# Kernel optimization log

Measured on AMD Instinct MI355X. Metric: run time of the kernel, lower is better.

## Reference

```python
import jax, jax.numpy as jnp
import numpy as np

N_HEAD = 16
NEG_INF = -1e30


def sparsemax(z):
    # sparsemax over last axis (Martins & Astudillo 2016)
    d = z.shape[-1]
    z_sorted = -jnp.sort(-z, axis=-1)                      # descending
    z_cumsum = jnp.cumsum(z_sorted, axis=-1)
    k = jnp.arange(1, d + 1, dtype=z.dtype)
    support = (1.0 + k * z_sorted) > z_cumsum
    rho = jnp.sum(support, axis=-1, keepdims=True)         # int, >=1
    rho_idx = jnp.clip(rho - 1, 0, None).astype(jnp.int32)
    cs_at_rho = jnp.take_along_axis(z_cumsum, rho_idx, axis=-1)
    tau = (cs_at_rho - 1.0) / jnp.maximum(rho.astype(z.dtype), 1.0)
    return jnp.clip(z - tau, 0.0, None)


def setup_inputs() -> dict:
    key = jax.random.key(0)
    ks = jax.random.split(key, 5)
    B, T, C = 4, 2048, 1024
    x = jax.random.normal(ks[0], (B, T, C), dtype=jnp.float32)
    W_attn = jax.random.normal(ks[1], (C, 3 * C), dtype=jnp.float32) * (1.0 / np.sqrt(C))
    b_attn = jax.random.normal(ks[2], (3 * C,), dtype=jnp.float32) * 0.01
    W_proj = jax.random.normal(ks[3], (C, C), dtype=jnp.float32) * (1.0 / np.sqrt(C))
    b_proj = jax.random.normal(ks[4], (C,), dtype=jnp.float32) * 0.01
    return {"x": x, "W_attn": W_attn, "b_attn": b_attn, "W_proj": W_proj, "b_proj": b_proj}


def reference(x, W_attn, b_attn, W_proj, b_proj):
    B, T, C = x.shape
    H = N_HEAD
    D = C // H
    qkv = x @ W_attn + b_attn                               # [B,T,3C]
    q, k, v = jnp.split(qkv, 3, axis=-1)
    q = q.reshape(B, T, H, D).transpose(0, 2, 1, 3)         # [B,H,T,D]
    k = k.reshape(B, T, H, D).transpose(0, 2, 1, 3)
    v = v.reshape(B, T, H, D).transpose(0, 2, 1, 3)
    # sparsemax over head dim of K (mode xsa_sparsemax_k)
    k = sparsemax(k)
    att = jnp.einsum('bhqd,bhkd->bhqk', q, k) * (1.0 / np.sqrt(D))
    causal = jnp.tril(jnp.ones((T, T), dtype=bool))
    att = jnp.where(causal[None, None], att, NEG_INF)
    att = jax.nn.softmax(att, axis=-1)
    y = jnp.einsum('bhqk,bhkd->bhqd', att, v)               # [B,H,T,D]
    # XSA output correction: subtract projection of y onto normalized v
    v_norm = jnp.sqrt(jnp.sum(v * v, axis=-1, keepdims=True))
    v_hat = v / jnp.maximum(v_norm, 1e-12)
    proj_coef = jnp.sum(y * v_hat, axis=-1, keepdims=True)
    y = y - proj_coef * v_hat
    y = y.transpose(0, 2, 1, 3).reshape(B, T, C)
    return y @ W_proj + b_proj
```

## Files before the change

### kernel.cpp

```cpp
#include <hip/hip_runtime.h>
#include <math.h>

#define NB 4
#define NH 16
#define TT 2048
#define CC 1024
#define DD 64
#define MM (NB * TT)

typedef __attribute__((ext_vector_type(8))) _Float16 half8;
typedef __attribute__((ext_vector_type(4))) _Float16 half4;
typedef __attribute__((ext_vector_type(4))) float floatx4;

__device__ __forceinline__ void gload16(const _Float16* g, _Float16* l) {
    auto gp = (const __attribute__((address_space(1))) void*)(uintptr_t)g;
    auto lp = (__attribute__((address_space(3))) void*)(uint32_t)(uintptr_t)l;
    __builtin_amdgcn_global_load_lds(gp, lp, 16, 0, 0);
}

__global__ __launch_bounds__(256) void split_x_kernel(
    const float* __restrict__ x, _Float16* __restrict__ xh,
    _Float16* __restrict__ xl)
{
    size_t i = ((size_t)blockIdx.x * 256 + threadIdx.x) * 4;
    float4 v = *(const float4*)&x[i];
    half4 h, l;
    h.x = (_Float16)v.x; l.x = (_Float16)(v.x - (float)h.x);
    h.y = (_Float16)v.y; l.y = (_Float16)(v.y - (float)h.y);
    h.z = (_Float16)v.z; l.z = (_Float16)(v.z - (float)h.z);
    h.w = (_Float16)v.w; l.w = (_Float16)(v.w - (float)h.w);
    *(half4*)&xh[i] = h;
    *(half4*)&xl[i] = l;
}

__global__ __launch_bounds__(256) void splitT_w_kernel(
    const float* __restrict__ W, _Float16* __restrict__ WhT,
    _Float16* __restrict__ WlT, int K, int N)
{
    __shared__ float Ls[64][65];
    const int bN = blockIdx.x * 64;
    const int bK = blockIdx.y * 64;
    const int tid = threadIdx.x;
    const int g = tid >> 4, c = tid & 15;

    #pragma unroll
    for (int u = 0; u < 4; u++) {
        int r = u * 16 + g;
        float4 v = *(const float4*)&W[(size_t)(bK + r) * N + bN + c * 4];
        Ls[r][c * 4 + 0] = v.x; Ls[r][c * 4 + 1] = v.y;
        Ls[r][c * 4 + 2] = v.z; Ls[r][c * 4 + 3] = v.w;
    }
    __syncthreads();
    #pragma unroll
    for (int u = 0; u < 4; u++) {
        int n = u * 16 + g;
        half4 h, l;
        float f;
        f = Ls[c * 4 + 0][n]; h.x = (_Float16)f; l.x = (_Float16)(f - (float)h.x);
        f = Ls[c * 4 + 1][n]; h.y = (_Float16)f; l.y = (_Float16)(f - (float)h.y);
        f = Ls[c * 4 + 2][n]; h.z = (_Float16)f; l.z = (_Float16)(f - (float)h.z);
        f = Ls[c * 4 + 3][n]; h.w = (_Float16)f; l.w = (_Float16)(f - (float)h.w);
        size_t o = (size_t)(bN + n) * K + bK + c * 4;
        *(half4*)&WhT[o] = h;
        *(half4*)&WlT[o] = l;
    }
}

__global__ __launch_bounds__(256) void gemm_ht3_kernel(
    const _Float16* __restrict__ Ah, const _Float16* __restrict__ Al,
    const _Float16* __restrict__ Bh, const _Float16* __restrict__ Bl,
    const float* __restrict__ bias, float* __restrict__ Cout,
    _Float16* __restrict__ outQh, _Float16* __restrict__ outQl,
    _Float16* __restrict__ outKh, _Float16* __restrict__ outKl,
    _Float16* __restrict__ outVt, int N, int K, int mode)
{
    __shared__ _Float16 sAh[128 * 32], sAl[128 * 32];
    __shared__ _Float16 sBh[128 * 32], sBl[128 * 32];

    const int bn = blockIdx.x * 128;
    const int bm = blockIdx.y * 128;
    const int tid = threadIdx.x;
    const int w = tid >> 6, lane = tid & 63;
    const int wm = (w >> 1) * 64, wn = (w & 1) * 64;

    const int rowS = w * 32 + (lane >> 2);
    const int kg = (lane & 3) * 8;
    const size_t offA0 = (size_t)(bm + rowS) * K + kg;
    const size_t offA1 = offA0 + (size_t)16 * K;
    const size_t offB0 = (size_t)(bn + rowS) * K + kg;
    const size_t offB1 = offB0 + (size_t)16 * K;
    const int ls0 = rowS * 32 + kg;
    const int ls1 = (rowS + 16) * 32 + kg;

    floatx4 acc[4][4];
    #pragma unroll
    for (int i = 0; i < 4; i++)
        #pragma unroll
        for (int j = 0; j < 4; j++)
            acc[i][j] = (floatx4){0.f, 0.f, 0.f, 0.f};

    const int fr = lane & 15, fq = (lane >> 4) * 8;

    for (int k0 = 0; k0 < K; k0 += 32) {
        __syncthreads();
        half8 a0 = *(const half8*)&Ah[offA0 + k0];
        half8 a1 = *(const half8*)&Ah[offA1 + k0];
        half8 a2 = *(const half8*)&Al[offA0 + k0];
        half8 a3 = *(const half8*)&Al[offA1 + k0];
        half8 b0 = *(const half8*)&Bh[offB0 + k0];
        half8 b1 = *(const half8*)&Bh[offB1 + k0];
        half8 b2 = *(const half8*)&Bl[offB0 + k0];
        half8 b3 = *(const half8*)&Bl[offB1 + k0];
        *(half8*)&sAh[ls0] = a0;
        *(half8*)&sAh[ls1] = a1;
        *(half8*)&sAl[ls0] = a2;
        *(half8*)&sAl[ls1] = a3;
        *(half8*)&sBh[ls0] = b0;
        *(half8*)&sBh[ls1] = b1;
        *(half8*)&sBl[ls0] = b2;
        *(half8*)&sBl[ls1] = b3;
        __syncthreads();

        half8 ah[4], al[4], bh[4], bl[4];
        #pragma unroll
        for (int t = 0; t < 4; t++) {
            ah[t] = *(const half8*)&sAh[(wm + t * 16 + fr) * 32 + fq];
            al[t] = *(const half8*)&sAl[(wm + t * 16 + fr) * 32 + fq];
            bh[t] = *(const half8*)&sBh[(wn + t * 16 + fr) * 32 + fq];
            bl[t] = *(const half8*)&sBl[(wn + t * 16 + fr) * 32 + fq];
        }
        #pragma unroll
        for (int mt = 0; mt < 4; mt++)
            #pragma unroll
            for (int nt = 0; nt < 4; nt++) {
                acc[mt][nt] = __builtin_amdgcn_mfma_f32_16x16x32_f16(
                    ah[mt], bh[nt], acc[mt][nt], 0, 0, 0);
                acc[mt][nt] = __builtin_amdgcn_mfma_f32_16x16x32_f16(
                    ah[mt], bl[nt], acc[mt][nt], 0, 0, 0);
                acc[mt][nt] = __builtin_amdgcn_mfma_f32_16x16x32_f16(
                    al[mt], bh[nt], acc[mt][nt], 0, 0, 0);
            }
    }

    const int col = lane & 15, row4 = (lane >> 4) * 4;
    if (mode == 0) {
        #pragma unroll
        for (int mt = 0; mt < 4; mt++)
            #pragma unroll
            for (int nt = 0; nt < 4; nt++) {
                const int n = bn + wn + nt * 16 + col;
                const float bv = bias[n];
                const int m0 = bm + wm + mt * 16 + row4;
                #pragma unroll
                for (int r = 0; r < 4; r++)
                    Cout[(size_t)(m0 + r) * N + n] = acc[mt][nt][r] + bv;
            }
    } else {
        #pragma unroll
        for (int mt = 0; mt < 4; mt++)
            #pragma unroll
            for (int nt = 0; nt < 4; nt++) {
                const int n = bn + wn + nt * 16 + col;
                const int which = n >> 10;
                const int cc_ = n & 1023;
                const int hh_ = cc_ >> 6, d = cc_ & 63;
                const int m0 = bm + wm + mt * 16 + row4;
                const int b = m0 >> 11, t0 = m0 & 2047;
                const size_t bhx = (size_t)b * NH + hh_;
                const float bv = bias[n];
                if (which == 0) {
                    #pragma unroll
                    for (int r = 0; r < 4; r++) {
                        const float qv = (acc[mt][nt][r] + bv) * 0.125f;
                        const _Float16 qh_ = (_Float16)qv;
                        const size_t o = (bhx * TT + t0 + r) * DD + d;
                        outQh[o] = qh_;
                        outQl[o] = (_Float16)(qv - (float)qh_);
                    }
                } else if (which == 1) {
                    #pragma unroll
                    for (int r = 0; r < 4; r++) {
                        const float kv = acc[mt][nt][r] + bv;
                        const _Float16 kh_ = (_Float16)kv;
                        const size_t o = (bhx * TT + t0 + r) * DD + d;
                        outKh[o] = kh_;
                        outKl[o] = (_Float16)(kv - (float)kh_);
                    }
                } else {
                    half4 vv;
                    #pragma unroll
                    for (int r = 0; r < 4; r++)
                        vv[r] = (_Float16)(acc[mt][nt][r] + bv);
                    *(half4*)&outVt[(bhx * DD + d) * TT + t0] = vv;
                }
            }
    }
}

__global__ __launch_bounds__(256) void sparsemax_kernel(
    _Float16* __restrict__ Kh, _Float16* __restrict__ Kl)
{
    const int lane = threadIdx.x & 63;
    const size_t row = (size_t)blockIdx.x * 4 + (threadIdx.x >> 6);
    const size_t off = row * DD + lane;
    float z = (float)Kh[off] + (float)Kl[off];
    float cnt = 0.f, ss = 0.f;
    #pragma unroll
    for (int j = 0; j < 64; j++) {
        float zj = __shfl(z, j, 64);
        if (zj >= z) { cnt += 1.f; ss += zj; }
    }
    float cond = (1.f + cnt * z > ss) ? 1.f : 0.f;
    float rho = cond, S = cond * z;
    #pragma unroll
    for (int o = 32; o; o >>= 1) {
        rho += __shfl_xor(rho, o, 64);
        S   += __shfl_xor(S,   o, 64);
    }
    float tau = (S - 1.f) / rho;
    float outv = fmaxf(z - tau, 0.f);
    _Float16 hh = (_Float16)outv;
    Kh[off] = hh;
    Kl[off] = (_Float16)(outv - (float)hh);
}

__global__ __launch_bounds__(256, 2) void attn_kernel(
    const _Float16* __restrict__ Qh, const _Float16* __restrict__ Ql,
    const _Float16* __restrict__ Kh, const _Float16* __restrict__ Kl,
    const _Float16* __restrict__ Vt,
    _Float16* __restrict__ Yh, _Float16* __restrict__ Yl)
{
    __shared__ _Float16 sKh[2][64 * DD];
    __shared__ _Float16 sKl[2][64 * DD];
    __shared__ _Float16 sV [2][64 * DD];

    const int tid = threadIdx.x;
    const int w = tid >> 6, lane = tid & 63;
    const int p = blockIdx.x >> 6;
    const int bhid = blockIdx.x & 63;
    const int b = bhid >> 4, h = bhid & 15;
    const size_t bh = (size_t)b * NH + h;
    const _Float16* Qhg = Qh + bh * (size_t)TT * DD;
    const _Float16* Qlg = Ql + bh * (size_t)TT * DD;
    const _Float16* Khg = Kh + bh * (size_t)TT * DD;
    const _Float16* Klg = Kl + bh * (size_t)TT * DD;
    const _Float16* Vtg = Vt + bh * (size_t)DD * TT;

    const int qrow = lane & 15;
    const int g = lane >> 4;
    const int swz = qrow & 7;
    const int sr = lane >> 3;
    const int uu = (lane & 7) ^ sr;

    auto stage = [&](int kt, int buf) {
        const int rb = w * 16;
        #pragma unroll
        for (int i = 0; i < 2; i++) {
            const int rr = rb + i * 8 + sr;
            const size_t ko = (size_t)(kt * 64 + rr) * DD + (uu << 3);
            gload16(&Khg[ko], &sKh[buf][(rb + i * 8) * DD]);
            gload16(&Klg[ko], &sKl[buf][(rb + i * 8) * DD]);
            gload16(&Vtg[(size_t)rr * TT + kt * 64 + (uu << 3)],
                    &sV[buf][(rb + i * 8) * DD]);
        }
    };

    const int qlist[2] = {p, 15 - p};
    int cur = 0;

    for (int qi = 0; qi < 2; qi++) {
        const int qt = qlist[qi];
        const int wq0 = qt * 128 + w * 32;
        const int wqmax = wq0 + 31;
        const int nkv = 2 * qt + 2;

        half8 qfh[2][2], qfl[2][2];
        #pragma unroll
        for (int nq = 0; nq < 2; nq++)
            #pragma unroll
            for (int ks = 0; ks < 2; ks++) {
                const size_t o = (size_t)(wq0 + nq * 16 + qrow) * DD
                               + (g << 3) + (ks << 5);
                qfh[nq][ks] = *(const half8*)&Qhg[o];
                qfl[nq][ks] = *(const half8*)&Qlg[o];
            }

        floatx4 acc[2][4];
        #pragma unroll
        for (int i = 0; i < 2; i++)
            #pragma unroll
            for (int j = 0; j < 4; j++)
                acc[i][j] = (floatx4){0.f, 0.f, 0.f, 0.f};
        float m_i[2] = {-3.0e38f, -3.0e38f};
        float l_i[2] = {0.f, 0.f};

        __syncthreads();
        stage(0, cur);

        for (int kt = 0; kt < nkv; kt++) {
            __syncthreads();
            if (kt + 1 < nkv) stage(kt + 1, cur ^ 1);

            if (kt * 64 <= wqmax) {
                const _Float16* kb = sKh[cur];
                const _Float16* lb = sKl[cur];
                const _Float16* vbp = sV[cur];

                floatx4 s[4][2];
                #pragma unroll
                for (int mk = 0; mk < 4; mk++)
                    #pragma unroll
                    for (int nq = 0; nq < 2; nq++)
                        s[mk][nq] = (floatx4){0.f, 0.f, 0.f, 0.f};

                #pragma unroll
                for (int mk = 0; mk < 4; mk++) {
                    #pragma unroll
                    for (int ks = 0; ks < 2; ks++) {
                        const int off = (qrow + mk * 16) * DD
                                      + (((g + (ks << 2)) ^ swz) << 3);
                        const half8 kfh = *(const half8*)&kb[off];
                        const half8 kfl = *(const half8*)&lb[off];
                        #pragma unroll
                        for (int nq = 0; nq < 2; nq++) {
                            s[mk][nq] = __builtin_amdgcn_mfma_f32_16x16x32_f16(
                                kfh, qfh[nq][ks], s[mk][nq], 0, 0, 0);
                            s[mk][nq] = __builtin_amdgcn_mfma_f32_16x16x32_f16(
                                kfh, qfl[nq][ks], s[mk][nq], 0, 0, 0);
                            s[mk][nq] = __builtin_amdgcn_mfma_f32_16x16x32_f16(
                                kfl, qfh[nq][ks], s[mk][nq], 0, 0, 0);
                        }
                    }
                }

                if (kt * 64 + 63 > wq0) {
                    #pragma unroll
                    for (int mk = 0; mk < 4; mk++)
                        #pragma unroll
                        for (int nq = 0; nq < 2; nq++)
                            #pragma unroll
                            for (int r = 0; r < 4; r++) {
                                const int kvg = kt * 64 + mk * 16 + (g << 2) + r;
                                const int qg  = wq0 + nq * 16 + qrow;
                                if (kvg > qg) s[mk][nq][r] = -1.0e30f;
                            }
                }

                float al_[2];
                #pragma unroll
                for (int nq = 0; nq < 2; nq++) {
                    float mx = s[0][nq][0];
                    #pragma unroll
                    for (int mk = 0; mk < 4; mk++)
                        #pragma unroll
                        for (int r = 0; r < 4; r++)
                            mx = fmaxf(mx, s[mk][nq][r]);
                    mx = fmaxf(mx, __shfl_xor(mx, 16, 64));
                    mx = fmaxf(mx, __shfl_xor(mx, 32, 64));
                    const float mn = fmaxf(m_i[nq], mx);
                    al_[nq] = __expf(m_i[nq] - mn);
                    m_i[nq] = mn;
                    float r0 = 0.f;
                    #pragma unroll
                    for (int mk = 0; mk < 4; mk++)
                        #pragma unroll
                        for (int r = 0; r < 4; r++) {
                            const float pp = __expf(s[mk][nq][r] - mn);
                            s[mk][nq][r] = pp;
                            r0 += pp;
                        }
                    r0 += __shfl_xor(r0, 16, 64);
                    r0 += __shfl_xor(r0, 32, 64);
                    l_i[nq] = l_i[nq] * al_[nq] + r0;
                }

                #pragma unroll
                for (int mt = 0; mt < 2; mt++)
                    #pragma unroll
                    for (int r = 0; r < 4; r++) {
                        const float aB = __shfl(al_[mt], (g << 2) | r, 64);
                        #pragma unroll
                        for (int nt = 0; nt < 4; nt++)
                            acc[mt][nt][r] *= aB;
                    }

                half4 ph[4][2], pl[4][2];
                #pragma unroll
                for (int mk = 0; mk < 4; mk++)
                    #pragma unroll
                    for (int nq = 0; nq < 2; nq++)
                        #pragma unroll
                        for (int r = 0; r < 4; r++) {
                            const float pv = s[mk][nq][r];
                            const _Float16 hh = (_Float16)pv;
                            ph[mk][nq][r] = hh;
                            pl[mk][nq][r] = (_Float16)(pv - (float)hh);
                        }

                #pragma unroll
                for (int mk = 0; mk < 4; mk++) {
                    #pragma unroll
                    for (int nt = 0; nt < 4; nt++) {
                        const int d = qrow + nt * 16;
                        const int u = ((mk << 1) | (g >> 1)) ^ swz;
                        const half4 vb = *(const half4*)
                            &vbp[d * DD + (u << 3) + ((g & 1) << 2)];
                        #pragma unroll
                        for (int nq = 0; nq < 2; nq++) {
                            acc[nq][nt] = __builtin_amdgcn_mfma_f32_16x16x16f16(
                                ph[mk][nq], vb, acc[nq][nt], 0, 0, 0);
                            acc[nq][nt] = __builtin_amdgcn_mfma_f32_16x16x16f16(
                                pl[mk][nq], vb, acc[nq][nt], 0, 0, 0);
                        }
                    }
                }
            }
            cur ^= 1;
        }

        #pragma unroll
        for (int mt = 0; mt < 2; mt++)
            #pragma unroll
            for (int r = 0; r < 4; r++) {
                const int qg = wq0 + mt * 16 + (g << 2) + r;
                const float invl = 1.0f / __shfl(l_i[mt], (g << 2) | r, 64);
                float y0 = acc[mt][0][r] * invl;
                float y1 = acc[mt][1][r] * invl;
                float y2 = acc[mt][2][r] * invl;
                float y3 = acc[mt][3][r] * invl;
                const float v0 = (float)Vtg[(size_t)qrow * TT + qg];
                const float v1 = (float)Vtg[(size_t)(qrow + 16) * TT + qg];
                const float v2 = (float)Vtg[(size_t)(qrow + 32) * TT + qg];
                const float v3 = (float)Vtg[(size_t)(qrow + 48) * TT + qg];
                float n2 = v0 * v0 + v1 * v1 + v2 * v2 + v3 * v3;
                #pragma unroll
                for (int o = 8; o; o >>= 1) n2 += __shfl_xor(n2, o, 64);
                const float ivn = 1.0f / fmaxf(sqrtf(n2), 1e-12f);
                float coef = y0 * v0 + y1 * v1 + y2 * v2 + y3 * v3;
                #pragma unroll
                for (int o = 8; o; o >>= 1) coef += __shfl_xor(coef, o, 64);
                coef *= ivn * ivn;
                const float o0 = y0 - coef * v0;
                const float o1 = y1 - coef * v1;
                const float o2 = y2 - coef * v2;
                const float o3 = y3 - coef * v3;
                const size_t ob = ((size_t)(b * TT + qg)) * CC + h * DD + qrow;
                _Float16 hh;
                hh = (_Float16)o0; Yh[ob]      = hh; Yl[ob]      = (_Float16)(o0 - (float)hh);
                hh = (_Float16)o1; Yh[ob + 16] = hh; Yl[ob + 16] = (_Float16)(o1 - (float)hh);
                hh = (_Float16)o2; Yh[ob + 32] = hh; Yl[ob + 32] = (_Float16)(o2 - (float)hh);
                hh = (_Float16)o3; Yh[ob + 48] = hh; Yl[ob + 48] = (_Float16)(o3 - (float)hh);
            }
    }
}

extern "C" void kernel_launch(void* const* d_in, const int* in_sizes, int n_in,
                              void* d_out, int out_size, void* d_ws, size_t ws_size,
                              hipStream_t stream) {
    const float* x      = (const float*)d_in[0];
    const float* W_attn = (const float*)d_in[1];
    const float* b_attn = (const float*)d_in[2];
    const float* W_proj = (const float*)d_in[3];
    const float* b_proj = (const float*)d_in[4];
    float* out = (float*)d_out;

    char* ws = (char*)d_ws;
    _Float16* xh   = (_Float16*)(ws);
    _Float16* xl   = (_Float16*)(ws + ((size_t)16 << 20));
    _Float16* WhT  = (_Float16*)(ws + ((size_t)32 << 20));
    _Float16* WlT  = (_Float16*)(ws + ((size_t)38 << 20));
    _Float16* Qh_  = (_Float16*)(ws + ((size_t)44 << 20));
    _Float16* Ql_  = (_Float16*)(ws + ((size_t)60 << 20));
    _Float16* Kh_  = (_Float16*)(ws + ((size_t)76 << 20));
    _Float16* Kl_  = (_Float16*)(ws + ((size_t)92 << 20));
    _Float16* Vt_  = (_Float16*)(ws + ((size_t)108 << 20));
    _Float16* Yh   = xh;
    _Float16* Yl   = xl;
    _Float16* WphT = WhT;
    _Float16* WplT = (_Float16*)(ws + ((size_t)34 << 20));

    split_x_kernel<<<(MM * CC) / (256 * 4), 256, 0, stream>>>(x, xh, xl);
    splitT_w_kernel<<<dim3(3 * CC / 64, CC / 64), 256, 0, stream>>>(
        W_attn, WhT, WlT, CC, 3 * CC);
    gemm_ht3_kernel<<<dim3(3 * CC / 128, MM / 128), 256, 0, stream>>>(
        xh, xl, WhT, WlT, b_attn, nullptr,
        Qh_, Ql_, Kh_, Kl_, Vt_, 3 * CC, CC, 1);
    sparsemax_kernel<<<dim3((NB * NH * TT) / 4), 256, 0, stream>>>(Kh_, Kl_);
    attn_kernel<<<dim3(512), 256, 0, stream>>>(Qh_, Ql_, Kh_, Kl_, Vt_, Yh, Yl);
    splitT_w_kernel<<<dim3(CC / 64, CC / 64), 256, 0, stream>>>(
        W_proj, WphT, WplT, CC, CC);
    gemm_ht3_kernel<<<dim3(CC / 128, MM / 128), 256, 0, stream>>>(
        Yh, Yl, WphT, WplT, b_proj, out,
        nullptr, nullptr, nullptr, nullptr, nullptr, CC, CC, 0);
}
```

Baseline: 551.7 us.

## Restructure split-fp16 GEMM with double-buffered async LDS loads and larger tiles

Rewrites the split-precision GEMM to use 512-thread blocks with a 128x256 tile, double-buffered LDS filled by global_load_lds direct-to-LDS loads, XOR-swizzled LDS layout to avoid bank conflicts, a grouped block-index swizzle for L2 reuse, and setprio around the MFMA burst. The goal is to overlap global loads with MFMA work and remove the register round-trip and one barrier per k-step. It raises LDS use and register pressure per block, which may limit occupancy.

```diff
diff --git a/kernel.cpp b/kernel.cpp
--- a/kernel.cpp
+++ b/kernel.cpp
@@ -7,6 +7,7 @@
 #define CC 1024
 #define DD 64
 #define MM (NB * TT)
+#define BK 32
 
 typedef __attribute__((ext_vector_type(8))) _Float16 half8;
 typedef __attribute__((ext_vector_type(4))) _Float16 half4;
@@ -66,31 +67,53 @@
     }
 }
 
-__global__ __launch_bounds__(256) void gemm_ht3_kernel(
+__global__ __launch_bounds__(512, 2) void gemm_ht3_kernel(
     const _Float16* __restrict__ Ah, const _Float16* __restrict__ Al,
     const _Float16* __restrict__ Bh, const _Float16* __restrict__ Bl,
     const float* __restrict__ bias, float* __restrict__ Cout,
     _Float16* __restrict__ outQh, _Float16* __restrict__ outQl,
     _Float16* __restrict__ outKh, _Float16* __restrict__ outKl,
-    _Float16* __restrict__ outVt, int N, int K, int mode)
+    _Float16* __restrict__ outVt, int N, int K, int nbx, int mode)
 {
-    __shared__ _Float16 sAh[128 * 32], sAl[128 * 32];
-    __shared__ _Float16 sBh[128 * 32], sBl[128 * 32];
-
-    const int bn = blockIdx.x * 128;
-    const int bm = blockIdx.y * 128;
+    __shared__ _Float16 sAh[2][128 * BK], sAl[2][128 * BK];
+    __shared__ _Float16 sBh[2][256 * BK], sBl[2][256 * BK];
+
+    const int nblk = gridDim.x;
+    const int id = blockIdx.x;
+    const int swzid = (id & 7) * (nblk >> 3) + (id >> 3);
+    const int by = swzid / nbx, bx = swzid - by * nbx;
+    const int bm = by * 128, bn = bx * 256;
+
     const int tid = threadIdx.x;
     const int w = tid >> 6, lane = tid & 63;
-    const int wm = (w >> 1) * 64, wn = (w & 1) * 64;
-
-    const int rowS = w * 32 + (lane >> 2);
-    const int kg = (lane & 3) * 8;
-    const size_t offA0 = (size_t)(bm + rowS) * K + kg;
-    const size_t offA1 = offA0 + (size_t)16 * K;
-    const size_t offB0 = (size_t)(bn + rowS) * K + kg;
-    const size_t offB1 = offB0 + (size_t)16 * K;
-    const int ls0 = rowS * 32 + kg;
-    const int ls1 = (rowS + 16) * 32 + kg;
+    const int wm = (w >> 2) * 64, wn = (w & 3) * 64;
+    const int fr = lane & 15, g = lane >> 4;
+
+    const int rS = w * 16 + (lane >> 2);
+    const int ug = ((lane & 3) ^ ((rS >> 1) & 3)) * 8;
+    const size_t gA  = (size_t)(bm + rS) * K + ug;
+    const size_t gB0 = (size_t)(bn + rS) * K + ug;
+    const size_t gB1 = (size_t)(bn + 128 + rS) * K + ug;
+    const int ldsW = w * 16 * BK;
+
+    auto stage = [&](int kt, int c) {
+        const int k0 = kt * BK;
+        gload16(&Ah[gA + k0],  &sAh[c][ldsW]);
+        gload16(&Al[gA + k0],  &sAl[c][ldsW]);
+        gload16(&Bh[gB0 + k0], &sBh[c][ldsW]);
+        gload16(&Bl[gB0 + k0], &sBl[c][ldsW]);
+        gload16(&Bh[gB1 + k0], &sBh[c][128 * BK + ldsW]);
+        gload16(&Bl[gB1 + k0], &sBl[c][128 * BK + ldsW]);
+    };
+
+    int offA[4], offB[4];
+    #pragma unroll
+    for (int t = 0; t < 4; t++) {
+        const int ra = wm + t * 16 + fr;
+        offA[t] = ra * BK + ((g ^ ((ra >> 1) & 3)) << 3);
+        const int rb = wn + t * 16 + fr;
+        offB[t] = rb * BK + ((g ^ ((rb >> 1) & 3)) << 3);
+    }
 
     floatx4 acc[4][4];
     #pragma unroll
@@ -99,50 +122,39 @@
         for (int j = 0; j < 4; j++)
             acc[i][j] = (floatx4){0.f, 0.f, 0.f, 0.f};
 
-    const int fr = lane & 15, fq = (lane >> 4) * 8;
-
-    for (int k0 = 0; k0 < K; k0 += 32) {
-        __syncthreads();
-        half8 a0 = *(const half8*)&Ah[offA0 + k0];
-        half8 a1 = *(const half8*)&Ah[offA1 + k0];
-        half8 a2 = *(const half8*)&Al[offA0 + k0];
-        half8 a3 = *(const half8*)&Al[offA1 + k0];
-        half8 b0 = *(const half8*)&Bh[offB0 + k0];
-        half8 b1 = *(const half8*)&Bh[offB1 + k0];
-        half8 b2 = *(const half8*)&Bl[offB0 + k0];
-        half8 b3 = *(const half8*)&Bl[offB1 + k0];
-        *(half8*)&sAh[ls0] = a0;
-        *(half8*)&sAh[ls1] = a1;
-        *(half8*)&sAl[ls0] = a2;
-        *(half8*)&sAl[ls1] = a3;
-        *(half8*)&sBh[ls0] = b0;
-        *(half8*)&sBh[ls1] = b1;
-        *(half8*)&sBl[ls0] = b2;
-        *(half8*)&sBl[ls1] = b3;
-        __syncthreads();
-
-        half8 ah[4], al[4], bh[4], bl[4];
+    stage(0, 0);
+    stage(1, 1);
+    __syncthreads();
+
+    const int NK = K >> 5;
+    for (int kt = 0; kt < NK; kt++) {
+        const int c = kt & 1;
+        half8 a_h[4], a_l[4], b_h[4], b_l[4];
         #pragma unroll
         for (int t = 0; t < 4; t++) {
-            ah[t] = *(const half8*)&sAh[(wm + t * 16 + fr) * 32 + fq];
-            al[t] = *(const half8*)&sAl[(wm + t * 16 + fr) * 32 + fq];
-            bh[t] = *(const half8*)&sBh[(wn + t * 16 + fr) * 32 + fq];
-            bl[t] = *(const half8*)&sBl[(wn + t * 16 + fr) * 32 + fq];
+            a_h[t] = *(const half8*)&sAh[c][offA[t]];
+            a_l[t] = *(const half8*)&sAl[c][offA[t]];
+            b_h[t] = *(const half8*)&sBh[c][offB[t]];
+            b_l[t] = *(const half8*)&sBl[c][offB[t]];
         }
+        __builtin_amdgcn_s_setprio(1);
         #pragma unroll
         for (int mt = 0; mt < 4; mt++)
             #pragma unroll
             for (int nt = 0; nt < 4; nt++) {
                 acc[mt][nt] = __builtin_amdgcn_mfma_f32_16x16x32_f16(
-                    ah[mt], bh[nt], acc[mt][nt], 0, 0, 0);
+                    a_h[mt], b_h[nt], acc[mt][nt], 0, 0, 0);
                 acc[mt][nt] = __builtin_amdgcn_mfma_f32_16x16x32_f16(
-                    ah[mt], bl[nt], acc[mt][nt], 0, 0, 0);
+                    a_h[mt], b_l[nt], acc[mt][nt], 0, 0, 0);
                 acc[mt][nt] = __builtin_amdgcn_mfma_f32_16x16x32_f16(
-                    al[mt], bh[nt], acc[mt][nt], 0, 0, 0);
+                    a_l[mt], b_h[nt], acc[mt][nt], 0, 0, 0);
             }
-    }
-
-    const int col = lane & 15, row4 = (lane >> 4) * 4;
+        __builtin_amdgcn_s_setprio(0);
+        __syncthreads();
+        if (kt + 2 < NK) stage(kt + 2, c);
+    }
+
+    const int col = lane & 15, row4 = g * 4;
     if (mode == 0) {
         #pragma unroll
         for (int mt = 0; mt < 4; mt++)
@@ -482,14 +494,14 @@
     split_x_kernel<<<(MM * CC) / (256 * 4), 256, 0, stream>>>(x, xh, xl);
     splitT_w_kernel<<<dim3(3 * CC / 64, CC / 64), 256, 0, stream>>>(
         W_attn, WhT, WlT, CC, 3 * CC);
-    gemm_ht3_kernel<<<dim3(3 * CC / 128, MM / 128), 256, 0, stream>>>(
+    gemm_ht3_kernel<<<dim3((MM / 128) * (3 * CC / 256)), 512, 0, stream>>>(
         xh, xl, WhT, WlT, b_attn, nullptr,
-        Qh_, Ql_, Kh_, Kl_, Vt_, 3 * CC, CC, 1);
+        Qh_, Ql_, Kh_, Kl_, Vt_, 3 * CC, CC, 3 * CC / 256, 1);
     sparsemax_kernel<<<dim3((NB * NH * TT) / 4), 256, 0, stream>>>(Kh_, Kl_);
     attn_kernel<<<dim3(512), 256, 0, stream>>>(Qh_, Ql_, Kh_, Kl_, Vt_, Yh, Yl);
     splitT_w_kernel<<<dim3(CC / 64, CC / 64), 256, 0, stream>>>(
         W_proj, WphT, WplT, CC, CC);
-    gemm_ht3_kernel<<<dim3(CC / 128, MM / 128), 256, 0, stream>>>(
+    gemm_ht3_kernel<<<dim3((MM / 128) * (CC / 256)), 512, 0, stream>>>(
         Yh, Yl, WphT, WplT, b_proj, out,
-        nullptr, nullptr, nullptr, nullptr, nullptr, CC, CC, 0);
-}
+        nullptr, nullptr, nullptr, nullptr, nullptr, CC, CC, CC / 256, 0);
+}
```

New measurement: 541.1 us. Within noise of the previous version (-1.9%).
